# Performance work log

Measured on AMD Instinct MI355X. Metric: run time of the kernel, lower is better.

Reference implementation:

```python
import jax, jax.numpy as jnp
import numpy as np

B, V = 256, 128000

def setup_inputs() -> dict:
    key = jax.random.key(0)
    k1, k2 = jax.random.split(key)
    logits = jax.random.normal(k1, (B, V), dtype=jnp.float32)
    # temperatures in [0.5, 1.5) to avoid degenerate near-zero temps
    temperatures = jax.random.uniform(k2, (B,), dtype=jnp.float32, minval=0.5, maxval=1.5)
    return {"logits": logits, "temperatures": temperatures, "top_k": 50}

def reference(logits, temperatures, top_k):
    # temperature scale (logits.float().div_(temps[:, None]))
    scaled = logits.astype(jnp.float32) / temperatures[:, None]          # [B, V]
    # top-k threshold: k-th largest value per row
    kth = jax.lax.top_k(scaled, top_k)[0][:, -1:]                        # [B, 1]
    # mask everything strictly below the k-th value to -inf
    masked = jnp.where(scaled < kth, -jnp.inf, scaled)                   # [B, V]
    # softmax + multinomial(1)  ==  categorical over masked logits
    samples = jax.random.categorical(jax.random.key(42), masked, axis=-1)  # [B]
    return samples
```

## Files before the change

kernel.cpp:

```cpp
#include <hip/hip_runtime.h>

#define T1 256
#define SPLIT 8
#define LDSCAP 1024
#define CAP_ROW 2048
#define OVF_BUMP (1u << 20)

#define T2 1024
#define BINS 4096
#define CAPF 4096
#define FLOOR_KEY 0xC0200000u
#define MARGIN 8u

__device__ __forceinline__ unsigned rotl32(unsigned x, unsigned r) {
  return (x << r) | (x >> (32u - r));
}

__device__ __forceinline__ unsigned threefry_xor_0_42(unsigned x0, unsigned x1) {
  const unsigned k0 = 0u, k1 = 42u, k2 = 0u ^ 42u ^ 0x1BD11BDAu;
  x0 += k0; x1 += k1;
#define TF_R(r) { x0 += x1; x1 = rotl32(x1, r); x1 ^= x0; }
  TF_R(13) TF_R(15) TF_R(26) TF_R(6)
  x0 += k1; x1 += k2 + 1u;
  TF_R(17) TF_R(29) TF_R(16) TF_R(24)
  x0 += k2; x1 += k0 + 2u;
  TF_R(13) TF_R(15) TF_R(26) TF_R(6)
  x0 += k0; x1 += k1 + 3u;
  TF_R(17) TF_R(29) TF_R(16) TF_R(24)
  x0 += k1; x1 += k2 + 4u;
  TF_R(13) TF_R(15) TF_R(26) TF_R(6)
  x0 += k2; x1 += k0 + 5u;
#undef TF_R
  return x0 ^ x1;
}

__device__ __forceinline__ float gumbel_at(unsigned flat) {
  unsigned bits = threefry_xor_0_42(0u, flat);
  float fl = __uint_as_float((bits >> 9) | 0x3F800000u) - 1.0f;
  const float tiny = 1.17549435e-38f;
  float u = fmaxf(fl + tiny, tiny);
  return -logf(-logf(u));
}

__device__ __forceinline__ unsigned f2k(float f) {
  unsigned b = __float_as_uint(f);
  return (b & 0x80000000u) ? ~b : (b ^ 0x80000000u);
}
__device__ __forceinline__ float k2f(unsigned k) {
  unsigned b = (k & 0x80000000u) ? (k ^ 0x80000000u) : ~k;
  return __uint_as_float(b);
}

__global__ __launch_bounds__(T1) void scan_kernel(
    const float* __restrict__ logits, unsigned* __restrict__ counters,
    unsigned* __restrict__ okeys, unsigned* __restrict__ oidxs, int V) {
  const int row = blockIdx.x / SPLIT;
  const int chunk = blockIdx.x - row * SPLIT;
  const int tid = threadIdx.x;
  const int nv4 = V >> 2;
  const int c4 = (nv4 + SPLIT - 1) / SPLIT;
  const int beg = chunk * c4;
  const int end = min(nv4, beg + c4);
  const float* rowp = logits + (size_t)row * (size_t)V;
  const float4* rowp4 = (const float4*)rowp;

  __shared__ unsigned skey[LDSCAP];
  __shared__ unsigned sidx[LDSCAP];
  __shared__ unsigned snc, sbase;
  if (tid == 0) snc = 0u;
  __syncthreads();

#pragma unroll 4
  for (int i = beg + tid; i < end; i += T1) {
    float4 v = rowp4[i];
    float f[4] = {v.x, v.y, v.z, v.w};
#pragma unroll
    for (int e = 0; e < 4; ++e) {
      unsigned key = f2k(f[e]);
      if (key >= FLOOR_KEY) {
        unsigned p = atomicAdd(&snc, 1u);
        if (p < LDSCAP) { skey[p] = key; sidx[p] = (unsigned)(i * 4 + e); }
      }
    }
  }
  if (chunk == SPLIT - 1) {
    for (int j = nv4 * 4 + tid; j < V; j += T1) {
      unsigned key = f2k(rowp[j]);
      if (key >= FLOOR_KEY) {
        unsigned p = atomicAdd(&snc, 1u);
        if (p < LDSCAP) { skey[p] = key; sidx[p] = (unsigned)j; }
      }
    }
  }
  __syncthreads();

  const unsigned nc = snc;
  const unsigned nb = min(nc, (unsigned)LDSCAP);
  if (tid == 0) {
    unsigned add = (nc > (unsigned)LDSCAP) ? (nb + OVF_BUMP) : nb;
    sbase = atomicAdd(&counters[row], add);
  }
  __syncthreads();
  const unsigned base = sbase;
  unsigned* kout = okeys + (size_t)row * CAP_ROW;
  unsigned* iout = oidxs + (size_t)row * CAP_ROW;
  for (unsigned p = tid; p < nb; p += T1) {
    unsigned g = base + p;
    if (g < (unsigned)CAP_ROW) { kout[g] = skey[p]; iout[g] = sidx[p]; }
  }
}

__global__ __launch_bounds__(T2) void select_kernel(
    const float* __restrict__ logits, const float* __restrict__ temps,
    const int* __restrict__ topk_ptr, const unsigned* __restrict__ counters,
    const unsigned* __restrict__ okeys, const unsigned* __restrict__ oidxs,
    int* __restrict__ out, int V) {
  const int row = blockIdx.x;
  const int tid = threadIdx.x;
  const unsigned K = (unsigned)(*topk_ptr);
  const float t = temps[row];
  const unsigned rowBase = (unsigned)row * (unsigned)V;
  const float* rowp = logits + (size_t)row * (size_t)V;
  const float4* rowp4 = (const float4*)rowp;
  const int nv4 = V >> 2;

  __shared__ unsigned hist[BINS];
  __shared__ unsigned cand_key[CAPF];
  __shared__ unsigned cand_idx[CAPF];
  __shared__ float    rv[T2];
  __shared__ unsigned ri[T2];
  __shared__ unsigned ncand, sBstar, sAbove, sK50;

  if (tid == 0) { ncand = 0u; sBstar = 0u; sAbove = 0u; sK50 = 0u; }
  __syncthreads();

  const unsigned cnt = counters[row];
  const bool tryFast = (cnt >= K && cnt <= (unsigned)CAP_ROW);
  unsigned c = 0;
  unsigned cntAbove = 0;

  if (tryFast) {
    c = cnt;
    const unsigned* kin = okeys + (size_t)row * CAP_ROW;
    const unsigned* iin = oidxs + (size_t)row * CAP_ROW;
    for (unsigned i = tid; i < c; i += T2) { cand_key[i] = kin[i]; cand_idx[i] = iin[i]; }
    __syncthreads();
    for (unsigned i = tid; i < c; i += T2) {
      unsigned ki = cand_key[i];
      unsigned gt = 0, eq = 0;
      for (unsigned j = 0; j < c; ++j) {
        unsigned kj = cand_key[j];
        gt += (kj > ki) ? 1u : 0u;
        eq += (kj == ki) ? 1u : 0u;
      }
      if (gt < K && gt + eq >= K) sK50 = ki;
    }
    __syncthreads();
  }

  const bool fastOK = tryFast && (sK50 >= FLOOR_KEY + MARGIN);

  float bestV = -INFINITY;
  unsigned bestI = 0xFFFFFFFFu;

  if (!fastOK) {
    for (int i = tid; i < BINS; i += T2) hist[i] = 0u;
    if (tid == 0) { ncand = 0u; sK50 = 0u; }
    __syncthreads();

    for (int i = tid; i < nv4; i += T2) {
      float4 v = rowp4[i];
      atomicAdd(&hist[f2k(v.x) >> 20], 1u);
      atomicAdd(&hist[f2k(v.y) >> 20], 1u);
      atomicAdd(&hist[f2k(v.z) >> 20], 1u);
      atomicAdd(&hist[f2k(v.w) >> 20], 1u);
    }
    for (int j = nv4 * 4 + tid; j < V; j += T2) atomicAdd(&hist[f2k(rowp[j]) >> 20], 1u);
    __syncthreads();

    if (tid < 64) {
      const int lane = tid;
      unsigned s = 0;
      for (int k = 0; k < 64; ++k) s += hist[lane * 64 + k];
      unsigned suf = s;
#pragma unroll
      for (int off = 1; off < 64; off <<= 1) {
        unsigned o = __shfl_down(suf, off);
        if (lane + off < 64) suf += o;
      }
      unsigned sufn = __shfl_down(suf, 1);
      if (lane == 63) sufn = 0u;
      if (suf >= K && sufn < K) {
        unsigned run = sufn;
        for (int k = 63; k >= 0; --k) {
          unsigned h = hist[lane * 64 + k];
          unsigned nr = run + h;
          if (run < K && nr >= K) { sBstar = (unsigned)(lane * 64 + k); sAbove = run; }
          run = nr;
        }
      }
    }
    __syncthreads();

    const unsigned Bstar = sBstar;
    cntAbove = sAbove;
    const unsigned long long binCeilP1 = ((unsigned long long)(Bstar + 1u)) << 20;
    const unsigned lowKey = (Bstar >= 1u) ? ((Bstar - 1u) << 20) : 0u;

    for (int i = tid; i < nv4; i += T2) {
      float4 v = rowp4[i];
      float f[4] = {v.x, v.y, v.z, v.w};
#pragma unroll
      for (int e = 0; e < 4; ++e) {
        unsigned key = f2k(f[e]);
        if (key < lowKey) continue;
        unsigned col = (unsigned)(i * 4 + e);
        if ((unsigned long long)key >= binCeilP1) {
          float sj = f[e] / t;
          float val = sj + gumbel_at(rowBase + col);
          if (val > bestV || (val == bestV && col < bestI)) { bestV = val; bestI = col; }
        } else {
          unsigned p = atomicAdd(&ncand, 1u);
          if (p < CAPF) { cand_key[p] = key; cand_idx[p] = col; }
        }
      }
    }
    for (int j = nv4 * 4 + tid; j < V; j += T2) {
      unsigned key = f2k(rowp[j]);
      if (key < lowKey) continue;
      if ((unsigned long long)key >= binCeilP1) {
        float sj = rowp[j] / t;
        float val = sj + gumbel_at(rowBase + (unsigned)j);
        if (val > bestV || (val == bestV && (unsigned)j < bestI)) { bestV = val; bestI = (unsigned)j; }
      } else {
        unsigned p = atomicAdd(&ncand, 1u);
        if (p < CAPF) { cand_key[p] = key; cand_idx[p] = (unsigned)j; }
      }
    }
    __syncthreads();

    c = min(ncand, (unsigned)CAPF);
    for (unsigned i = tid; i < c; i += T2) {
      unsigned ki = cand_key[i];
      unsigned gt = 0, eq = 0;
      for (unsigned j = 0; j < c; ++j) {
        unsigned kj = cand_key[j];
        gt += (kj > ki) ? 1u : 0u;
        eq += (kj == ki) ? 1u : 0u;
      }
      if (cntAbove + gt < K && cntAbove + gt + eq >= K) sK50 = ki;
    }
    __syncthreads();
  }

  const float s50 = k2f(sK50) / t;
  for (unsigned i = tid; i < c; i += T2) {
    unsigned col = cand_idx[i];
    if (col >= (unsigned)V) continue;
    float sj = k2f(cand_key[i]) / t;
    if (sj >= s50) {
      float val = sj + gumbel_at(rowBase + col);
      if (val > bestV || (val == bestV && col < bestI)) { bestV = val; bestI = col; }
    }
  }

  rv[tid] = bestV; ri[tid] = bestI;
  __syncthreads();
  for (int off = T2 / 2; off > 0; off >>= 1) {
    if (tid < off) {
      float v2 = rv[tid + off]; unsigned i2 = ri[tid + off];
      if (v2 > rv[tid] || (v2 == rv[tid] && i2 < ri[tid])) { rv[tid] = v2; ri[tid] = i2; }
    }
    __syncthreads();
  }
  if (tid == 0) out[row] = (int)((ri[0] < (unsigned)V) ? ri[0] : 0u);
}

extern "C" void kernel_launch(void* const* d_in, const int* in_sizes, int n_in,
                              void* d_out, int out_size, void* d_ws, size_t ws_size,
                              hipStream_t stream) {
  const float* logits = (const float*)d_in[0];
  const float* temps  = (const float*)d_in[1];
  const int*   topk   = (const int*)d_in[2];
  int* out = (int*)d_out;

  const int B = in_sizes[1];
  const int V = in_sizes[0] / B;

  unsigned* counters = (unsigned*)d_ws;
  unsigned* okeys = counters + B;
  unsigned* oidxs = okeys + (size_t)B * CAP_ROW;

  hipMemsetAsync(counters, 0, (size_t)B * sizeof(unsigned), stream);
  scan_kernel<<<B * SPLIT, T1, 0, stream>>>(logits, counters, okeys, oidxs, V);
  select_kernel<<<B, T2, 0, stream>>>(logits, temps, topk, counters, okeys, oidxs, out, V);
}
```

Measured before the change: 227.4 us.

## Use per-chunk candidate slots instead of global atomics and drop memset

Each scan block now writes its candidates to a fixed per-chunk slot and records its count, and the select kernel prefix-sums the eight counts to gather them. This removes the global atomic counter and the memset launch. The scan loop is also manually unrolled to four float4 loads per iteration, uses a cheaper unsigned-range test on the raw bits for the floor check, and sets a launch-bounds occupancy hint. The workspace grows to B*SPLIT*LDSCAP entries, and the fast path now accepts up to CAPF candidates.

```diff
diff --git a/kernel.cpp b/kernel.cpp
--- a/kernel.cpp
+++ b/kernel.cpp
@@ -3,13 +3,14 @@
 #define T1 256
 #define SPLIT 8
 #define LDSCAP 1024
-#define CAP_ROW 2048
-#define OVF_BUMP (1u << 20)
+#define OVF_MARK 0xFFFFFFFFu
 
 #define T2 1024
 #define BINS 4096
 #define CAPF 4096
 #define FLOOR_KEY 0xC0200000u
+#define FLOOR_BITS 0x40200000u
+#define FLOOR_RANGE 0x3FE00000u
 #define MARGIN 8u
 
 __device__ __forceinline__ unsigned rotl32(unsigned x, unsigned r) {
@@ -51,11 +52,11 @@
   return __uint_as_float(b);
 }
 
-__global__ __launch_bounds__(T1) void scan_kernel(
-    const float* __restrict__ logits, unsigned* __restrict__ counters,
+__global__ __launch_bounds__(T1, 8) void scan_kernel(
+    const float* __restrict__ logits, unsigned* __restrict__ counts,
     unsigned* __restrict__ okeys, unsigned* __restrict__ oidxs, int V) {
-  const int row = blockIdx.x / SPLIT;
-  const int chunk = blockIdx.x - row * SPLIT;
+  const int row = blockIdx.x >> 3;
+  const int chunk = blockIdx.x & (SPLIT - 1);
   const int tid = threadIdx.x;
   const int nv4 = V >> 2;
   const int c4 = (nv4 + SPLIT - 1) / SPLIT;
@@ -66,53 +67,47 @@
 
   __shared__ unsigned skey[LDSCAP];
   __shared__ unsigned sidx[LDSCAP];
-  __shared__ unsigned snc, sbase;
+  __shared__ unsigned snc;
   if (tid == 0) snc = 0u;
   __syncthreads();
 
-#pragma unroll 4
-  for (int i = beg + tid; i < end; i += T1) {
-    float4 v = rowp4[i];
-    float f[4] = {v.x, v.y, v.z, v.w};
-#pragma unroll
-    for (int e = 0; e < 4; ++e) {
-      unsigned key = f2k(f[e]);
-      if (key >= FLOOR_KEY) {
-        unsigned p = atomicAdd(&snc, 1u);
-        if (p < LDSCAP) { skey[p] = key; sidx[p] = (unsigned)(i * 4 + e); }
-      }
-    }
-  }
+#define TEST1(vv, col) do {                                              \
+    unsigned b_ = __float_as_uint(vv);                                   \
+    if (__builtin_expect(b_ - FLOOR_BITS < FLOOR_RANGE, 0)) {            \
+      unsigned p_ = atomicAdd(&snc, 1u);                                 \
+      if (p_ < LDSCAP) { skey[p_] = b_ ^ 0x80000000u; sidx[p_] = (unsigned)(col); } \
+    } } while (0)
+#define TEST4(vv, i4) do {                                               \
+    TEST1((vv).x, (i4) * 4 + 0); TEST1((vv).y, (i4) * 4 + 1);            \
+    TEST1((vv).z, (i4) * 4 + 2); TEST1((vv).w, (i4) * 4 + 3); } while (0)
+
+  int i = beg + tid;
+  for (; i + 3 * T1 < end; i += 4 * T1) {
+    float4 v0 = rowp4[i];
+    float4 v1 = rowp4[i + T1];
+    float4 v2 = rowp4[i + 2 * T1];
+    float4 v3 = rowp4[i + 3 * T1];
+    TEST4(v0, i); TEST4(v1, i + T1); TEST4(v2, i + 2 * T1); TEST4(v3, i + 3 * T1);
+  }
+  for (; i < end; i += T1) { float4 v = rowp4[i]; TEST4(v, i); }
   if (chunk == SPLIT - 1) {
-    for (int j = nv4 * 4 + tid; j < V; j += T1) {
-      unsigned key = f2k(rowp[j]);
-      if (key >= FLOOR_KEY) {
-        unsigned p = atomicAdd(&snc, 1u);
-        if (p < LDSCAP) { skey[p] = key; sidx[p] = (unsigned)j; }
-      }
-    }
-  }
+    for (int j = nv4 * 4 + tid; j < V; j += T1) TEST1(rowp[j], j);
+  }
+#undef TEST4
+#undef TEST1
   __syncthreads();
 
   const unsigned nc = snc;
   const unsigned nb = min(nc, (unsigned)LDSCAP);
-  if (tid == 0) {
-    unsigned add = (nc > (unsigned)LDSCAP) ? (nb + OVF_BUMP) : nb;
-    sbase = atomicAdd(&counters[row], add);
-  }
-  __syncthreads();
-  const unsigned base = sbase;
-  unsigned* kout = okeys + (size_t)row * CAP_ROW;
-  unsigned* iout = oidxs + (size_t)row * CAP_ROW;
-  for (unsigned p = tid; p < nb; p += T1) {
-    unsigned g = base + p;
-    if (g < (unsigned)CAP_ROW) { kout[g] = skey[p]; iout[g] = sidx[p]; }
-  }
+  if (tid == 0) counts[row * SPLIT + chunk] = (nc > (unsigned)LDSCAP) ? OVF_MARK : nc;
+  unsigned* kout = okeys + (size_t)(row * SPLIT + chunk) * LDSCAP;
+  unsigned* iout = oidxs + (size_t)(row * SPLIT + chunk) * LDSCAP;
+  for (unsigned p = tid; p < nb; p += T1) { kout[p] = skey[p]; iout[p] = sidx[p]; }
 }
 
 __global__ __launch_bounds__(T2) void select_kernel(
     const float* __restrict__ logits, const float* __restrict__ temps,
-    const int* __restrict__ topk_ptr, const unsigned* __restrict__ counters,
+    const int* __restrict__ topk_ptr, const unsigned* __restrict__ counts,
     const unsigned* __restrict__ okeys, const unsigned* __restrict__ oidxs,
     int* __restrict__ out, int V) {
   const int row = blockIdx.x;
@@ -129,21 +124,42 @@
   __shared__ unsigned cand_idx[CAPF];
   __shared__ float    rv[T2];
   __shared__ unsigned ri[T2];
+  __shared__ unsigned soff[SPLIT + 1];
+  __shared__ int      sovf;
   __shared__ unsigned ncand, sBstar, sAbove, sK50;
 
-  if (tid == 0) { ncand = 0u; sBstar = 0u; sAbove = 0u; sK50 = 0u; }
+  if (tid == 0) {
+    ncand = 0u; sBstar = 0u; sAbove = 0u; sK50 = 0u;
+    unsigned s = 0; int ovf = 0;
+    const unsigned* c8 = counts + row * SPLIT;
+#pragma unroll
+    for (int cch = 0; cch < SPLIT; ++cch) {
+      unsigned n = c8[cch];
+      if (n == OVF_MARK) { ovf = 1; n = 0u; }
+      soff[cch] = s; s += n;
+    }
+    soff[SPLIT] = s; sovf = ovf;
+  }
   __syncthreads();
 
-  const unsigned cnt = counters[row];
-  const bool tryFast = (cnt >= K && cnt <= (unsigned)CAP_ROW);
+  const unsigned total = soff[SPLIT];
+  const bool tryFast = (!sovf && total >= K && total <= (unsigned)CAPF);
   unsigned c = 0;
   unsigned cntAbove = 0;
 
   if (tryFast) {
-    c = cnt;
-    const unsigned* kin = okeys + (size_t)row * CAP_ROW;
-    const unsigned* iin = oidxs + (size_t)row * CAP_ROW;
-    for (unsigned i = tid; i < c; i += T2) { cand_key[i] = kin[i]; cand_idx[i] = iin[i]; }
+    c = total;
+#pragma unroll
+    for (int cch = 0; cch < SPLIT; ++cch) {
+      const unsigned off = soff[cch];
+      const unsigned nbc = soff[cch + 1] - off;
+      const unsigned* kin = okeys + (size_t)(row * SPLIT + cch) * LDSCAP;
+      const unsigned* iin = oidxs + (size_t)(row * SPLIT + cch) * LDSCAP;
+      for (unsigned p = tid; p < nbc; p += T2) {
+        cand_key[off + p] = kin[p];
+        cand_idx[off + p] = iin[p];
+      }
+    }
     __syncthreads();
     for (unsigned i = tid; i < c; i += T2) {
       unsigned ki = cand_key[i];
@@ -287,11 +303,10 @@
   const int B = in_sizes[1];
   const int V = in_sizes[0] / B;
 
-  unsigned* counters = (unsigned*)d_ws;
-  unsigned* okeys = counters + B;
-  unsigned* oidxs = okeys + (size_t)B * CAP_ROW;
-
-  hipMemsetAsync(counters, 0, (size_t)B * sizeof(unsigned), stream);
-  scan_kernel<<<B * SPLIT, T1, 0, stream>>>(logits, counters, okeys, oidxs, V);
-  select_kernel<<<B, T2, 0, stream>>>(logits, temps, topk, counters, okeys, oidxs, out, V);
-}
+  unsigned* counts = (unsigned*)d_ws;
+  unsigned* okeys = counts + (size_t)B * SPLIT;
+  unsigned* oidxs = okeys + (size_t)B * SPLIT * LDSCAP;
+
+  scan_kernel<<<B * SPLIT, T1, 0, stream>>>(logits, counts, okeys, oidxs, V);
+  select_kernel<<<B, T2, 0, stream>>>(logits, temps, topk, counts, okeys, oidxs, out, V);
+}
```

After: 228.2 us. No clear change (+0.3%).
